# Optimization experiments

Hardware: AMD Instinct MI355X
Metric: run time of the kernel (lower is better)

## Reference

```python
import jax, jax.numpy as jnp
import numpy as np

EPS = 1e-6
ROPE_BASE = 10000.0

def setup_inputs() -> dict:
    key = jax.random.key(0)
    ks = jax.random.split(key, 6)
    B, S, D = 4, 4096, 1024
    NS, DS = 4, D // 4          # num_subspaces, subspace_dim
    H = 2 * DS                  # hidden_dim = ff_multiplier * subspace_dim
    scale = 0.02
    return {
        "x": jax.random.normal(ks[0], (B, S, D), dtype=jnp.float32),
        "norm_w": jnp.ones((D,), dtype=jnp.float32),
        # grouped SwiGLU weights: [NS, in, out] layout so we can einsum directly
        "Wg": jax.random.normal(ks[1], (NS, DS, H), dtype=jnp.float32) * scale,
        "Wu": jax.random.normal(ks[2], (NS, DS, H), dtype=jnp.float32) * scale,
        "Wd": jax.random.normal(ks[3], (NS, H, DS), dtype=jnp.float32) * scale,
        "Wo": jax.random.normal(ks[4], (D, D), dtype=jnp.float32) * scale,
    }

def _rope_cos_sin(S, D, dtype):
    inv_freq = 1.0 / (ROPE_BASE ** (jnp.arange(0, D, 2, dtype=jnp.float32) / D))
    freqs = jnp.arange(S, dtype=jnp.float32)[:, None] * inv_freq[None, :]  # [S, D/2]
    emb = jnp.concatenate([freqs, freqs], axis=-1)                          # [S, D]
    return jnp.cos(emb).astype(dtype), jnp.sin(emb).astype(dtype)

def reference(x, norm_w, Wg, Wu, Wd, Wo):
    B, S, D = x.shape
    NS, DS, H = Wg.shape
    # RMSNorm
    h = x * jax.lax.rsqrt(jnp.mean(x * x, axis=-1, keepdims=True) + EPS) * norm_w
    # RoPE over full hidden dim (rotate_half convention)
    cos, sin = _rope_cos_sin(S, D, x.dtype)
    half = D // 2
    rot = jnp.concatenate([-h[..., half:], h[..., :half]], axis=-1)
    h = h * cos[None] + rot * sin[None]
    # Grouped SwiGLU over NS independent subspaces
    hc = h.reshape(B, S, NS, DS)
    gate = jax.nn.silu(jnp.einsum('bsnd,ndh->bsnh', hc, Wg))
    up = jnp.einsum('bsnd,ndh->bsnh', hc, Wu)
    down = jnp.einsum('bsnh,nhd->bsnd', gate * up, Wd)
    out = down.reshape(B, S, D)
    # Final projection + residual
    return jnp.einsum('bsd,de->bse', out, Wo) + x
```

## Files before the change

kernel.cpp:

```cpp
#include <hip/hip_runtime.h>

typedef unsigned short u16;
typedef unsigned int   u32;

typedef float  f32x4  __attribute__((ext_vector_type(4)));
typedef __bf16 bf16x8 __attribute__((ext_vector_type(8)));

#define S_LEN  4096
#define DMODEL 1024
#define NSUB   4
#define DSUB   256
#define HFF    512
#define NTOK   16384

static_assert(sizeof(bf16x8) == 16, "frag size");

__device__ __forceinline__ u16 f2bf(float f) {
    union { float f; u32 u; } v; v.f = f;
    u32 r = (v.u + 0x7fffu + ((v.u >> 16) & 1u)) >> 16;
    return (u16)r;
}

#define MFMA16(a, b, c) __builtin_amdgcn_mfma_f32_16x16x32_bf16((a), (b), (c), 0, 0, 0)

__device__ __forceinline__ void gl_lds16(const void* g, void* l) {
    __builtin_amdgcn_global_load_lds(
        (const __attribute__((address_space(1))) void*)g,
        (__attribute__((address_space(3))) void*)l,
        16, 0, 0);
}
#define LGKM0 asm volatile("s_waitcnt lgkmcnt(0)" ::: "memory")
#define SCHED0 __builtin_amdgcn_sched_barrier(0)
#define SBAR __builtin_amdgcn_s_barrier()

__global__ __launch_bounds__(256) void k_repack_all(const float* __restrict__ Wg,
                                                    const float* __restrict__ Wu,
                                                    const float* __restrict__ Wd,
                                                    const float* __restrict__ Wo,
                                                    u16* __restrict__ wgP,
                                                    u16* __restrict__ wuP,
                                                    u16* __restrict__ wdP,
                                                    u16* __restrict__ woP) {
    __shared__ float tl[32][65];
    int bid = blockIdx.x;
    const float* src; u16* dst; int K, C, rel;
    if (bid < 256)      { src = Wg; dst = wgP; K = 256;  C = 512;  rel = bid; }
    else if (bid < 512) { src = Wu; dst = wuP; K = 256;  C = 512;  rel = bid - 256; }
    else if (bid < 768) { src = Wd; dst = wdP; K = 512;  C = 256;  rel = bid - 512; }
    else                { src = Wo; dst = woP; K = 1024; C = 1024; rel = bid - 768; }
    int ncb = C >> 6, nkt = K >> 5;
    int cb = rel % ncb; int r2 = rel / ncb;
    int kt = r2 % nkt;  int b  = r2 / nkt;

    int tid = threadIdx.x;
    {
        int r = tid >> 3, c0 = (tid & 7) * 8;
        const float* s = src + ((size_t)(b * K + kt * 32 + r)) * C + cb * 64 + c0;
        float4 v0 = *(const float4*)(s);
        float4 v1 = *(const float4*)(s + 4);
        tl[r][c0 + 0] = v0.x; tl[r][c0 + 1] = v0.y; tl[r][c0 + 2] = v0.z; tl[r][c0 + 3] = v0.w;
        tl[r][c0 + 4] = v1.x; tl[r][c0 + 5] = v1.y; tl[r][c0 + 6] = v1.z; tl[r][c0 + 7] = v1.w;
    }
    __syncthreads();
    {
        int f = tid >> 6, l = tid & 63;
        union { u16 v[8]; uint4 q; } u;
#pragma unroll
        for (int j = 0; j < 8; ++j)
            u.v[j] = f2bf(tl[(l >> 4) * 8 + j][f * 16 + (l & 15)]);
        size_t ctile = (size_t)(b * (C >> 4) + cb * 4 + f);
        *(uint4*)(dst + (ctile * nkt + kt) * 512 + l * 8) = u.q;
    }
}

__global__ __launch_bounds__(256) void k_norm_rope(const float* __restrict__ x,
                                                   const float* __restrict__ nw,
                                                   u16* __restrict__ h) {
    int tok = blockIdx.x;
    int s = tok & (S_LEN - 1);
    int t = threadIdx.x;
    const float* xr = x + (size_t)tok * DMODEL;
    float x0 = xr[t], x1 = xr[t + 256], x2 = xr[t + 512], x3 = xr[t + 768];
    float ss = x0 * x0 + x1 * x1 + x2 * x2 + x3 * x3;
#pragma unroll
    for (int o = 32; o > 0; o >>= 1) ss += __shfl_down(ss, o, 64);
    __shared__ float red[4];
    if ((t & 63) == 0) red[t >> 6] = ss;
    __syncthreads();
    float tot = red[0] + red[1] + red[2] + red[3];
    float sc = rsqrtf(tot * (1.0f / DMODEL) + 1e-6f);
    float n0 = x0 * sc * nw[t];
    float n1 = x1 * sc * nw[t + 256];
    float n2 = x2 * sc * nw[t + 512];
    float n3 = x3 * sc * nw[t + 768];
    const float C = -0.017988946039015984f;
    float sf = (float)s;
    float ang0 = sf * expf(C * (float)t);
    float ang1 = sf * expf(C * (float)(t + 256));
    float sn0, cs0, sn1, cs1;
    sincosf(ang0, &sn0, &cs0);
    sincosf(ang1, &sn1, &cs1);
    u16* hr = h + (size_t)tok * DMODEL;
    hr[t]       = f2bf(n0 * cs0 - n2 * sn0);
    hr[t + 256] = f2bf(n1 * cs1 - n3 * sn1);
    hr[t + 512] = f2bf(n2 * cs0 + n0 * sn0);
    hr[t + 768] = f2bf(n3 * cs1 + n1 * sn1);
}

__global__ __launch_bounds__(512, 2)
void k_swiglu(const u16* __restrict__ h,
              const u16* __restrict__ wgP,
              const u16* __restrict__ wuP,
              const u16* __restrict__ wdP,
              u16* __restrict__ dmid) {
    int bid = blockIdx.x;
    int mb = bid & 255, n = bid >> 8;
    int m0 = mb * 64;
    int tid = threadIdx.x;
    int lane = tid & 63, wid = tid >> 6;

    __shared__ u16 hA[64 * 256];
    __shared__ u16 sT[64 * 128];
    __shared__ u16 sW[8 * 2 * 1024];

    const u16* wg = wgP + (size_t)n * (32 * 8 * 512);
    const u16* wu = wuP + (size_t)n * (32 * 8 * 512);
    const u16* wd = wdP + (size_t)n * (16 * 16 * 512);
    u16* myW = sW + wid * 2048;

#define ISSUE(t)                                                               \
    do {                                                                       \
        if ((t) < 48) {                                                        \
            const int hcs = (t) / 12, rs = (t) % 12;                           \
            u16* db = myW + ((t) % 2) * 1024;                                  \
            if (rs < 8) {                                                      \
                size_t ct0 = (size_t)(hcs * 8 + wid);                          \
                gl_lds16(wg + (ct0 * 8 + rs) * 512 + lane * 8, db);            \
                gl_lds16(wu + (ct0 * 8 + rs) * 512 + lane * 8, db + 512);      \
            } else {                                                           \
                const int k2s = rs - 8;                                        \
                gl_lds16(wd + ((size_t)(wid * 2 + 0) * 16 + hcs * 4 + k2s) * 512 + lane * 8, db);        \
                gl_lds16(wd + ((size_t)(wid * 2 + 1) * 16 + hcs * 4 + k2s) * 512 + lane * 8, db + 512);  \
            }                                                                  \
        }                                                                      \
    } while (0)
#define VMW(t)                                                                 \
    do {                                                                       \
        if ((t) <= 46) asm volatile("s_waitcnt vmcnt(2)" ::: "memory");        \
        else           asm volatile("s_waitcnt vmcnt(0)" ::: "memory");        \
    } while (0)

    const u16* hbase = h + (size_t)m0 * DMODEL + n * DSUB;
    uint4 hv[4];
#pragma unroll
    for (int it = 0; it < 4; ++it) {
        int e = (tid + it * 512) * 8;
        int r = e >> 8, c = e & 255;
        hv[it] = *(const uint4*)(hbase + (size_t)r * DMODEL + c);
    }
    ISSUE(0); ISSUE(1);
#pragma unroll
    for (int it = 0; it < 4; ++it) {
        int e = (tid + it * 512) * 8;
        int r = e >> 8, c = e & 255;
        u32 off = ((u32)(r * 512 + c * 2)) ^ ((u32)(r & 7) << 4);
        *(uint4*)((char*)hA + off) = hv[it];
    }
    LGKM0; SBAR;

    const f32x4 zero = {0.f, 0.f, 0.f, 0.f};
    f32x4 accd[4][2];
#pragma unroll
    for (int a = 0; a < 4; ++a) { accd[a][0] = zero; accd[a][1] = zero; }

#pragma unroll
    for (int hc = 0; hc < 4; ++hc) {
        f32x4 accg[4], accu[4];
#pragma unroll
        for (int a = 0; a < 4; ++a) { accg[a] = zero; accu[a] = zero; }

#pragma unroll
        for (int ks = 0; ks < 8; ++ks) {
            const int t = hc * 12 + ks;
            VMW(t); SCHED0;
            const u16* rb = myW + (t % 2) * 1024;
            bf16x8 bg = *(const bf16x8*)(rb + lane * 8);
            bf16x8 bu = *(const bf16x8*)(rb + 512 + lane * 8);
            LGKM0; SCHED0;
            ISSUE(t + 2);
#pragma unroll
            for (int rt = 0; rt < 4; ++rt) {
                int arow = rt * 16 + (lane & 15);
                int k0 = ks * 32 + (lane >> 4) * 8;
                u32 off = ((u32)(arow * 512 + k0 * 2)) ^ ((u32)(arow & 7) << 4);
                bf16x8 afr = *(const bf16x8*)((const char*)hA + off);
                accg[rt] = MFMA16(afr, bg, accg[rt]);
                accu[rt] = MFMA16(afr, bu, accu[rt]);
            }
        }

#pragma unroll
        for (int rt = 0; rt < 4; ++rt) {
            int rbase = rt * 16 + (lane >> 4) * 4;
            int col = wid * 16 + (lane & 15);
#pragma unroll
            for (int q = 0; q < 4; ++q) {
                float g = accg[rt][q], u = accu[rt][q];
                float tv = (g / (1.0f + __expf(-g))) * u;
                int row = rbase + q;
                u32 off = ((u32)(row * 256 + col * 2)) ^ ((u32)(row & 7) << 4);
                *(u16*)((char*)sT + off) = f2bf(tv);
            }
        }
        LGKM0; SBAR;

#pragma unroll
        for (int k2 = 0; k2 < 4; ++k2) {
            const int t = hc * 12 + 8 + k2;
            VMW(t); SCHED0;
            const u16* rb = myW + (t % 2) * 1024;
            bf16x8 bd0 = *(const bf16x8*)(rb + lane * 8);
            bf16x8 bd1 = *(const bf16x8*)(rb + 512 + lane * 8);
            LGKM0; SCHED0;
            ISSUE(t + 2);
#pragma unroll
            for (int rt = 0; rt < 4; ++rt) {
                int arow = rt * 16 + (lane & 15);
                int k0 = k2 * 32 + (lane >> 4) * 8;
                u32 off = ((u32)(arow * 256 + k0 * 2)) ^ ((u32)(arow & 7) << 4);
                bf16x8 afr = *(const bf16x8*)((const char*)sT + off);
                accd[rt][0] = MFMA16(afr, bd0, accd[rt][0]);
                accd[rt][1] = MFMA16(afr, bd1, accd[rt][1]);
            }
        }
        LGKM0; SBAR;
    }
#undef ISSUE
#undef VMW

#pragma unroll
    for (int rt = 0; rt < 4; ++rt)
#pragma unroll
        for (int ct = 0; ct < 2; ++ct) {
            int rbase = m0 + rt * 16 + (lane >> 4) * 4;
            int col = n * DSUB + wid * 32 + ct * 16 + (lane & 15);
#pragma unroll
            for (int q = 0; q < 4; ++q)
                dmid[(size_t)(rbase + q) * DMODEL + col] = f2bf(accd[rt][ct][q]);
        }
}

__global__ __launch_bounds__(512, 2) void k_final(const u16* __restrict__ dmid,
                                                  const u16* __restrict__ woP,
                                                  const float* __restrict__ x,
                                                  float* __restrict__ out) {
    int bid = blockIdx.x;
    int mb = bid & 127, nb = bid >> 7;
    int m0 = mb * 128, n0 = nb * 256;
    int tid = threadIdx.x;
    int lane = tid & 63, wid = tid >> 6;
    int wr = wid >> 2, wc = wid & 3;

    __shared__ u16 sA[2][128 * 256];

    f32x4 acc[4][4];
    const u16* dbase = dmid + (size_t)m0 * DMODEL;

    uint4 stA[8], stB[8];
#pragma unroll
    for (int it = 0; it < 8; ++it) {
        int e = (tid + it * 512) * 8;
        int r = e >> 8, c = e & 255;
        stA[it] = *(const uint4*)(dbase + (size_t)r * DMODEL + c);
    }
#pragma unroll
    for (int rt = 0; rt < 4; ++rt)
#pragma unroll
        for (int ct = 0; ct < 4; ++ct) {
            int rbase = m0 + wr * 64 + rt * 16 + (lane >> 4) * 4;
            int col = n0 + wc * 64 + ct * 16 + (lane & 15);
#pragma unroll
            for (int q = 0; q < 4; ++q)
                acc[rt][ct][q] = x[(size_t)(rbase + q) * DMODEL + col];
        }
#pragma unroll
    for (int it = 0; it < 8; ++it) {
        int e = (tid + it * 512) * 8;
        int r = e >> 8, c = e & 255;
        u32 off = ((u32)(r * 512 + c * 2)) ^ ((u32)(r & 7) << 4);
        *(uint4*)((char*)sA[0] + off) = stA[it];
    }
#pragma unroll
    for (int it = 0; it < 8; ++it) {
        int e = (tid + it * 512) * 8;
        int r = e >> 8, c = e & 255;
        stB[it] = *(const uint4*)(dbase + (size_t)r * DMODEL + 256 + c);
    }

#pragma unroll
    for (int kc = 0; kc < 4; ++kc) {
        __syncthreads();
        if (kc < 3) {
#pragma unroll
            for (int it = 0; it < 8; ++it) {
                int e = (tid + it * 512) * 8;
                int r = e >> 8, c = e & 255;
                u32 off = ((u32)(r * 512 + c * 2)) ^ ((u32)(r & 7) << 4);
                uint4 v = (kc & 1) ? stA[it] : stB[it];
                *(uint4*)((char*)sA[(kc + 1) & 1] + off) = v;
            }
        }
        if (kc < 2) {
#pragma unroll
            for (int it = 0; it < 8; ++it) {
                int e = (tid + it * 512) * 8;
                int r = e >> 8, c = e & 255;
                uint4 v = *(const uint4*)(dbase + (size_t)r * DMODEL + (kc + 2) * 256 + c);
                if ((kc & 1) == 0) stA[it] = v; else stB[it] = v;
            }
        }

        const u16* sAc = (const u16*)sA[kc & 1];
        bf16x8 wf[2][4];
#pragma unroll
        for (int ct = 0; ct < 4; ++ct) {
            size_t ctile = (size_t)(nb * 16 + wc * 4 + ct);
            size_t ktile = (size_t)(kc * 8 + 0);
            wf[0][ct] = *(const bf16x8*)(woP + (ctile * 32 + ktile) * 512 + lane * 8);
        }
#pragma unroll
        for (int ks = 0; ks < 8; ++ks) {
            if (ks < 7) {
#pragma unroll
                for (int ct = 0; ct < 4; ++ct) {
                    size_t ctile = (size_t)(nb * 16 + wc * 4 + ct);
                    size_t ktile = (size_t)(kc * 8 + ks + 1);
                    wf[(ks + 1) & 1][ct] = *(const bf16x8*)(woP + (ctile * 32 + ktile) * 512 + lane * 8);
                }
            }
            bf16x8 afr[4];
#pragma unroll
            for (int rt = 0; rt < 4; ++rt) {
                int arow = wr * 64 + rt * 16 + (lane & 15);
                int k0 = ks * 32 + (lane >> 4) * 8;
                u32 off = ((u32)(arow * 512 + k0 * 2)) ^ ((u32)(arow & 7) << 4);
                afr[rt] = *(const bf16x8*)((const char*)sAc + off);
            }
#pragma unroll
            for (int ct = 0; ct < 4; ++ct)
#pragma unroll
                for (int rt = 0; rt < 4; ++rt)
                    acc[rt][ct] = MFMA16(afr[rt], wf[ks & 1][ct], acc[rt][ct]);
        }
    }

#pragma unroll
    for (int rt = 0; rt < 4; ++rt)
#pragma unroll
        for (int ct = 0; ct < 4; ++ct) {
            int rbase = m0 + wr * 64 + rt * 16 + (lane >> 4) * 4;
            int col = n0 + wc * 64 + ct * 16 + (lane & 15);
#pragma unroll
            for (int q = 0; q < 4; ++q) {
                size_t o = (size_t)(rbase + q) * DMODEL + col;
                out[o] = acc[rt][ct][q];
            }
        }
}

extern "C" void kernel_launch(void* const* d_in, const int* in_sizes, int n_in,
                              void* d_out, int out_size, void* d_ws, size_t ws_size,
                              hipStream_t stream) {
    const float* x  = (const float*)d_in[0];
    const float* nw = (const float*)d_in[1];
    const float* Wg = (const float*)d_in[2];
    const float* Wu = (const float*)d_in[3];
    const float* Wd = (const float*)d_in[4];
    const float* Wo = (const float*)d_in[5];
    float* out = (float*)d_out;

    char* ws = (char*)d_ws;
    const size_t MB = 1u << 20;
    u16* h    = (u16*)(ws);
    u16* wgP  = (u16*)(ws + 32 * MB);
    u16* wuP  = (u16*)(ws + 33 * MB);
    u16* wdP  = (u16*)(ws + 34 * MB);
    u16* woP  = (u16*)(ws + 35 * MB);
    u16* dmid = (u16*)(ws + 37 * MB);

    k_repack_all<<<1280, 256, 0, stream>>>(Wg, Wu, Wd, Wo, wgP, wuP, wdP, woP);
    k_norm_rope<<<NTOK, 256, 0, stream>>>(x, nw, h);
    k_swiglu<<<256 * NSUB, 512, 0, stream>>>(h, wgP, wuP, wdP, dmid);
    k_final<<<128 * 4, 512, 0, stream>>>(dmid, woP, x, out);
}
```

Baseline: 177.7 us.

## Merge prep kernels and load SwiGLU weights directly into registers with double-buffered sT

Fuses the weight-repack and norm+RoPE kernels into a single launch, which removes one kernel boundary. In the SwiGLU kernel, weight fragments are no longer staged through LDS with async global_load_lds. They are now loaded straight from global memory into registers with one-step software prefetch. The sT intermediate is double-buffered so the trailing barrier after the down-projection can be dropped. This trades the explicit async pipeline for simpler register prefetch, which may expose global load latency and raise register pressure.

```diff
diff --git a/kernel.cpp b/kernel.cpp
--- a/kernel.cpp
+++ b/kernel.cpp
@@ -23,62 +23,52 @@
 
 #define MFMA16(a, b, c) __builtin_amdgcn_mfma_f32_16x16x32_bf16((a), (b), (c), 0, 0, 0)
 
-__device__ __forceinline__ void gl_lds16(const void* g, void* l) {
-    __builtin_amdgcn_global_load_lds(
-        (const __attribute__((address_space(1))) void*)g,
-        (__attribute__((address_space(3))) void*)l,
-        16, 0, 0);
-}
-#define LGKM0 asm volatile("s_waitcnt lgkmcnt(0)" ::: "memory")
-#define SCHED0 __builtin_amdgcn_sched_barrier(0)
-#define SBAR __builtin_amdgcn_s_barrier()
-
-__global__ __launch_bounds__(256) void k_repack_all(const float* __restrict__ Wg,
-                                                    const float* __restrict__ Wu,
-                                                    const float* __restrict__ Wd,
-                                                    const float* __restrict__ Wo,
-                                                    u16* __restrict__ wgP,
-                                                    u16* __restrict__ wuP,
-                                                    u16* __restrict__ wdP,
-                                                    u16* __restrict__ woP) {
-    __shared__ float tl[32][65];
+__global__ __launch_bounds__(256) void k_prep(const float* __restrict__ Wg,
+                                              const float* __restrict__ Wu,
+                                              const float* __restrict__ Wd,
+                                              const float* __restrict__ Wo,
+                                              const float* __restrict__ x,
+                                              const float* __restrict__ nw,
+                                              u16* __restrict__ wgP,
+                                              u16* __restrict__ wuP,
+                                              u16* __restrict__ wdP,
+                                              u16* __restrict__ woP,
+                                              u16* __restrict__ h) {
     int bid = blockIdx.x;
-    const float* src; u16* dst; int K, C, rel;
-    if (bid < 256)      { src = Wg; dst = wgP; K = 256;  C = 512;  rel = bid; }
-    else if (bid < 512) { src = Wu; dst = wuP; K = 256;  C = 512;  rel = bid - 256; }
-    else if (bid < 768) { src = Wd; dst = wdP; K = 512;  C = 256;  rel = bid - 512; }
-    else                { src = Wo; dst = woP; K = 1024; C = 1024; rel = bid - 768; }
-    int ncb = C >> 6, nkt = K >> 5;
-    int cb = rel % ncb; int r2 = rel / ncb;
-    int kt = r2 % nkt;  int b  = r2 / nkt;
-
     int tid = threadIdx.x;
-    {
-        int r = tid >> 3, c0 = (tid & 7) * 8;
-        const float* s = src + ((size_t)(b * K + kt * 32 + r)) * C + cb * 64 + c0;
-        float4 v0 = *(const float4*)(s);
-        float4 v1 = *(const float4*)(s + 4);
-        tl[r][c0 + 0] = v0.x; tl[r][c0 + 1] = v0.y; tl[r][c0 + 2] = v0.z; tl[r][c0 + 3] = v0.w;
-        tl[r][c0 + 4] = v1.x; tl[r][c0 + 5] = v1.y; tl[r][c0 + 6] = v1.z; tl[r][c0 + 7] = v1.w;
-    }
-    __syncthreads();
-    {
-        int f = tid >> 6, l = tid & 63;
-        union { u16 v[8]; uint4 q; } u;
-#pragma unroll
-        for (int j = 0; j < 8; ++j)
-            u.v[j] = f2bf(tl[(l >> 4) * 8 + j][f * 16 + (l & 15)]);
-        size_t ctile = (size_t)(b * (C >> 4) + cb * 4 + f);
-        *(uint4*)(dst + (ctile * nkt + kt) * 512 + l * 8) = u.q;
-    }
-}
-
-__global__ __launch_bounds__(256) void k_norm_rope(const float* __restrict__ x,
-                                                   const float* __restrict__ nw,
-                                                   u16* __restrict__ h) {
-    int tok = blockIdx.x;
+    if (bid < 1280) {
+        __shared__ float tl[32][65];
+        const float* src; u16* dst; int K, C, rel;
+        if (bid < 256)      { src = Wg; dst = wgP; K = 256;  C = 512;  rel = bid; }
+        else if (bid < 512) { src = Wu; dst = wuP; K = 256;  C = 512;  rel = bid - 256; }
+        else if (bid < 768) { src = Wd; dst = wdP; K = 512;  C = 256;  rel = bid - 512; }
+        else                { src = Wo; dst = woP; K = 1024; C = 1024; rel = bid - 768; }
+        int ncb = C >> 6, nkt = K >> 5;
+        int cb = rel % ncb; int r2 = rel / ncb;
+        int kt = r2 % nkt;  int b  = r2 / nkt;
+        {
+            int r = tid >> 3, c0 = (tid & 7) * 8;
+            const float* s = src + ((size_t)(b * K + kt * 32 + r)) * C + cb * 64 + c0;
+            float4 v0 = *(const float4*)(s);
+            float4 v1 = *(const float4*)(s + 4);
+            tl[r][c0 + 0] = v0.x; tl[r][c0 + 1] = v0.y; tl[r][c0 + 2] = v0.z; tl[r][c0 + 3] = v0.w;
+            tl[r][c0 + 4] = v1.x; tl[r][c0 + 5] = v1.y; tl[r][c0 + 6] = v1.z; tl[r][c0 + 7] = v1.w;
+        }
+        __syncthreads();
+        {
+            int f = tid >> 6, l = tid & 63;
+            union { u16 v[8]; uint4 q; } u;
+#pragma unroll
+            for (int j = 0; j < 8; ++j)
+                u.v[j] = f2bf(tl[(l >> 4) * 8 + j][f * 16 + (l & 15)]);
+            size_t ctile = (size_t)(b * (C >> 4) + cb * 4 + f);
+            *(uint4*)(dst + (ctile * nkt + kt) * 512 + l * 8) = u.q;
+        }
+        return;
+    }
+    int tok = bid - 1280;
     int s = tok & (S_LEN - 1);
-    int t = threadIdx.x;
+    int t = tid;
     const float* xr = x + (size_t)tok * DMODEL;
     float x0 = xr[t], x1 = xr[t + 256], x2 = xr[t + 512], x3 = xr[t + 768];
     float ss = x0 * x0 + x1 * x1 + x2 * x2 + x3 * x3;
@@ -120,53 +110,22 @@
     int lane = tid & 63, wid = tid >> 6;
 
     __shared__ u16 hA[64 * 256];
-    __shared__ u16 sT[64 * 128];
-    __shared__ u16 sW[8 * 2 * 1024];
+    __shared__ u16 sT[2][64 * 128];
 
     const u16* wg = wgP + (size_t)n * (32 * 8 * 512);
     const u16* wu = wuP + (size_t)n * (32 * 8 * 512);
     const u16* wd = wdP + (size_t)n * (16 * 16 * 512);
-    u16* myW = sW + wid * 2048;
-
-#define ISSUE(t)                                                               \
-    do {                                                                       \
-        if ((t) < 48) {                                                        \
-            const int hcs = (t) / 12, rs = (t) % 12;                           \
-            u16* db = myW + ((t) % 2) * 1024;                                  \
-            if (rs < 8) {                                                      \
-                size_t ct0 = (size_t)(hcs * 8 + wid);                          \
-                gl_lds16(wg + (ct0 * 8 + rs) * 512 + lane * 8, db);            \
-                gl_lds16(wu + (ct0 * 8 + rs) * 512 + lane * 8, db + 512);      \
-            } else {                                                           \
-                const int k2s = rs - 8;                                        \
-                gl_lds16(wd + ((size_t)(wid * 2 + 0) * 16 + hcs * 4 + k2s) * 512 + lane * 8, db);        \
-                gl_lds16(wd + ((size_t)(wid * 2 + 1) * 16 + hcs * 4 + k2s) * 512 + lane * 8, db + 512);  \
-            }                                                                  \
-        }                                                                      \
-    } while (0)
-#define VMW(t)                                                                 \
-    do {                                                                       \
-        if ((t) <= 46) asm volatile("s_waitcnt vmcnt(2)" ::: "memory");        \
-        else           asm volatile("s_waitcnt vmcnt(0)" ::: "memory");        \
-    } while (0)
 
     const u16* hbase = h + (size_t)m0 * DMODEL + n * DSUB;
-    uint4 hv[4];
 #pragma unroll
     for (int it = 0; it < 4; ++it) {
         int e = (tid + it * 512) * 8;
         int r = e >> 8, c = e & 255;
-        hv[it] = *(const uint4*)(hbase + (size_t)r * DMODEL + c);
-    }
-    ISSUE(0); ISSUE(1);
-#pragma unroll
-    for (int it = 0; it < 4; ++it) {
-        int e = (tid + it * 512) * 8;
-        int r = e >> 8, c = e & 255;
+        uint4 v = *(const uint4*)(hbase + (size_t)r * DMODEL + c);
         u32 off = ((u32)(r * 512 + c * 2)) ^ ((u32)(r & 7) << 4);
-        *(uint4*)((char*)hA + off) = hv[it];
-    }
-    LGKM0; SBAR;
+        *(uint4*)((char*)hA + off) = v;
+    }
+    __syncthreads();
 
     const f32x4 zero = {0.f, 0.f, 0.f, 0.f};
     f32x4 accd[4][2];
@@ -179,26 +138,28 @@
 #pragma unroll
         for (int a = 0; a < 4; ++a) { accg[a] = zero; accu[a] = zero; }
 
+        size_t ct0 = (size_t)(hc * 8 + wid);
+        bf16x8 bg[2], bu[2];
+        bg[0] = *(const bf16x8*)(wg + (ct0 * 8 + 0) * 512 + lane * 8);
+        bu[0] = *(const bf16x8*)(wu + (ct0 * 8 + 0) * 512 + lane * 8);
 #pragma unroll
         for (int ks = 0; ks < 8; ++ks) {
-            const int t = hc * 12 + ks;
-            VMW(t); SCHED0;
-            const u16* rb = myW + (t % 2) * 1024;
-            bf16x8 bg = *(const bf16x8*)(rb + lane * 8);
-            bf16x8 bu = *(const bf16x8*)(rb + 512 + lane * 8);
-            LGKM0; SCHED0;
-            ISSUE(t + 2);
+            if (ks < 7) {
+                bg[(ks + 1) & 1] = *(const bf16x8*)(wg + (ct0 * 8 + ks + 1) * 512 + lane * 8);
+                bu[(ks + 1) & 1] = *(const bf16x8*)(wu + (ct0 * 8 + ks + 1) * 512 + lane * 8);
+            }
 #pragma unroll
             for (int rt = 0; rt < 4; ++rt) {
                 int arow = rt * 16 + (lane & 15);
                 int k0 = ks * 32 + (lane >> 4) * 8;
                 u32 off = ((u32)(arow * 512 + k0 * 2)) ^ ((u32)(arow & 7) << 4);
                 bf16x8 afr = *(const bf16x8*)((const char*)hA + off);
-                accg[rt] = MFMA16(afr, bg, accg[rt]);
-                accu[rt] = MFMA16(afr, bu, accu[rt]);
-            }
-        }
-
+                accg[rt] = MFMA16(afr, bg[ks & 1], accg[rt]);
+                accu[rt] = MFMA16(afr, bu[ks & 1], accu[rt]);
+            }
+        }
+
+        u16* sTc = (u16*)sT[hc & 1];
 #pragma unroll
         for (int rt = 0; rt < 4; ++rt) {
             int rbase = rt * 16 + (lane >> 4) * 4;
@@ -209,34 +170,31 @@
                 float tv = (g / (1.0f + __expf(-g))) * u;
                 int row = rbase + q;
                 u32 off = ((u32)(row * 256 + col * 2)) ^ ((u32)(row & 7) << 4);
-                *(u16*)((char*)sT + off) = f2bf(tv);
-            }
-        }
-        LGKM0; SBAR;
-
+                *(u16*)((char*)sTc + off) = f2bf(tv);
+            }
+        }
+        __syncthreads();
+
+        bf16x8 bdA[2], bdB[2];
+        bdA[0] = *(const bf16x8*)(wd + ((size_t)(wid * 2 + 0) * 16 + hc * 4 + 0) * 512 + lane * 8);
+        bdB[0] = *(const bf16x8*)(wd + ((size_t)(wid * 2 + 1) * 16 + hc * 4 + 0) * 512 + lane * 8);
 #pragma unroll
         for (int k2 = 0; k2 < 4; ++k2) {
-            const int t = hc * 12 + 8 + k2;
-            VMW(t); SCHED0;
-            const u16* rb = myW + (t % 2) * 1024;
-            bf16x8 bd0 = *(const bf16x8*)(rb + lane * 8);
-            bf16x8 bd1 = *(const bf16x8*)(rb + 512 + lane * 8);
-            LGKM0; SCHED0;
-            ISSUE(t + 2);
+            if (k2 < 3) {
+                bdA[(k2 + 1) & 1] = *(const bf16x8*)(wd + ((size_t)(wid * 2 + 0) * 16 + hc * 4 + k2 + 1) * 512 + lane * 8);
+                bdB[(k2 + 1) & 1] = *(const bf16x8*)(wd + ((size_t)(wid * 2 + 1) * 16 + hc * 4 + k2 + 1) * 512 + lane * 8);
+            }
 #pragma unroll
             for (int rt = 0; rt < 4; ++rt) {
                 int arow = rt * 16 + (lane & 15);
                 int k0 = k2 * 32 + (lane >> 4) * 8;
                 u32 off = ((u32)(arow * 256 + k0 * 2)) ^ ((u32)(arow & 7) << 4);
-                bf16x8 afr = *(const bf16x8*)((const char*)sT + off);
-                accd[rt][0] = MFMA16(afr, bd0, accd[rt][0]);
-                accd[rt][1] = MFMA16(afr, bd1, accd[rt][1]);
-            }
-        }
-        LGKM0; SBAR;
-    }
-#undef ISSUE
-#undef VMW
+                bf16x8 afr = *(const bf16x8*)((const char*)sTc + off);
+                accd[rt][0] = MFMA16(afr, bdA[k2 & 1], accd[rt][0]);
+                accd[rt][1] = MFMA16(afr, bdB[k2 & 1], accd[rt][1]);
+            }
+        }
+    }
 
 #pragma unroll
     for (int rt = 0; rt < 4; ++rt)
@@ -388,8 +346,8 @@
     u16* woP  = (u16*)(ws + 35 * MB);
     u16* dmid = (u16*)(ws + 37 * MB);
 
-    k_repack_all<<<1280, 256, 0, stream>>>(Wg, Wu, Wd, Wo, wgP, wuP, wdP, woP);
-    k_norm_rope<<<NTOK, 256, 0, stream>>>(x, nw, h);
+    k_prep<<<1280 + NTOK, 256, 0, stream>>>(Wg, Wu, Wd, Wo, x, nw,
+                                            wgP, wuP, wdP, woP, h);
     k_swiglu<<<256 * NSUB, 512, 0, stream>>>(h, wgP, wuP, wdP, dmid);
     k_final<<<128 * 4, 512, 0, stream>>>(dmid, woP, x, out);
 }
```

New measurement: 181.4 us. 2.0% more time.
